# Performance work log

Measured on AMD Instinct MI355X. Metric: run time of the kernel, lower is better.

Reference implementation:

```python
import jax, jax.numpy as jnp
import numpy as np

B, N, C_IN = 2, 2048, 256
H, C_H = 8, 32  # no_heads, c_hidden; H*C_H == 256


def setup_inputs() -> dict:
    key = jax.random.key(0)
    ks = jax.random.split(key, 10)
    s_in = 1.0 / np.sqrt(C_IN)
    s_hid = 1.0 / np.sqrt(H * C_H)
    return {
        "q_x": jax.random.normal(ks[0], (B, N, C_IN), dtype=jnp.float32),
        "kv_x": jax.random.normal(ks[1], (B, N, C_IN), dtype=jnp.float32),
        "bias": jax.random.normal(ks[2], (B, H, N, N), dtype=jnp.float32),
        # Linear weights stored as [in, out] (transpose of torch layout)
        "Wq": jax.random.normal(ks[3], (C_IN, H * C_H), dtype=jnp.float32) * s_in,
        "Wk": jax.random.normal(ks[4], (C_IN, H * C_H), dtype=jnp.float32) * s_in,
        "Wv": jax.random.normal(ks[5], (C_IN, H * C_H), dtype=jnp.float32) * s_in,
        "Wg": jax.random.normal(ks[6], (C_IN, H * C_H), dtype=jnp.float32) * s_in,
        "bg": jnp.zeros((H * C_H,), dtype=jnp.float32),
        "Wo": jax.random.normal(ks[7], (H * C_H, C_IN), dtype=jnp.float32) * s_hid,
        "bo": jnp.zeros((C_IN,), dtype=jnp.float32),
    }


def reference(q_x, kv_x, bias, Wq, Wk, Wv, Wg, bg, Wo, bo):
    inv_sqrt = 1.0 / jnp.sqrt(jnp.asarray(C_H, q_x.dtype))
    # projections -> [B, N, H, C_H]
    q = (q_x @ Wq).reshape(B, N, H, C_H) * inv_sqrt
    k = (kv_x @ Wk).reshape(B, N, H, C_H)
    v = (kv_x @ Wv).reshape(B, N, H, C_H)
    # attention scores [B, H, Nq, Nk] with added pairwise bias
    a = jnp.einsum("bqhc,bkhc->bhqk", q, k) + bias
    a = jax.nn.softmax(a, axis=-1)
    o = jnp.einsum("bhqk,bkhc->bqhc", a, v)  # [B, N, H, C_H]
    # sigmoid gating
    g = jax.nn.sigmoid(q_x @ Wg + bg).reshape(B, N, H, C_H)
    o = o * g
    # output projection
    return o.reshape(B, N, H * C_H) @ Wo + bo
```

## Files before the change

kernel.cpp:

```cpp
#include <hip/hip_runtime.h>
#include <hip/hip_bf16.h>

#define B_   2
#define N_   2048
#define CIN  256
#define NH   8
#define CH   32

typedef unsigned short u16;
typedef __attribute__((ext_vector_type(4))) float f32x4;
typedef __bf16 bf16x8 __attribute__((ext_vector_type(8)));
typedef u16 u16x4 __attribute__((ext_vector_type(4)));
typedef u16 u16x8 __attribute__((ext_vector_type(8)));

static __device__ __forceinline__ u16 b16(float f) {
    __bf16 h = (__bf16)f;
    union { __bf16 h; u16 u; } c; c.h = h; return c.u;
}
static __device__ __forceinline__ float bf2f(u16 u) {
    union { unsigned u; float f; } c; c.u = ((unsigned)u) << 16; return c.f;
}
static __device__ __forceinline__ float sigmoidf_(float x) {
    return 1.0f / (1.0f + __expf(-x));
}
static __device__ __forceinline__ void gload_lds16(const void* g, void* lds) {
    __builtin_amdgcn_global_load_lds(
        (const __attribute__((address_space(1))) unsigned int*)g,
        (__attribute__((address_space(3))) unsigned int*)lds, 16, 0, 0);
}

#define LDW 136

static __device__ __forceinline__ u16x8 cvt8(float4 a, float4 b) {
    u16x8 o;
    o[0] = b16(a.x); o[1] = b16(a.y); o[2] = b16(a.z); o[3] = b16(a.w);
    o[4] = b16(b.x); o[5] = b16(b.y); o[6] = b16(b.z); o[7] = b16(b.w);
    return o;
}
static __device__ __forceinline__ void stg_b16(const u16* __restrict__ src, u16 (*dst)[LDW], int tid) {
#pragma unroll
    for (int i = 0; i < 4; i++) {
        const int e = tid + 256 * i, row = e >> 4, c = e & 15;
        *(bf16x8*)&dst[row][c * 8] = *(const bf16x8*)(src + (size_t)row * CIN + c * 8);
    }
}
static __device__ __forceinline__ void ld1_b16(const u16* __restrict__ src, bf16x8 r[4], int tid) {
#pragma unroll
    for (int i = 0; i < 4; i++) {
        const int e = tid + 256 * i, row = e >> 4, c = e & 15;
        r[i] = *(const bf16x8*)(src + (size_t)row * CIN + 128 + c * 8);
    }
}
static __device__ __forceinline__ void wr1_b16(const bf16x8 r[4], u16 (*dst)[LDW], int tid) {
#pragma unroll
    for (int i = 0; i < 4; i++) {
        const int e = tid + 256 * i, row = e >> 4, c = e & 15;
        *(bf16x8*)&dst[row][c * 8] = r[i];
    }
}
static __device__ __forceinline__ void stg_f32(const float* __restrict__ src, u16 (*dst)[LDW], int tid) {
#pragma unroll
    for (int i = 0; i < 4; i++) {
        const int e = tid + 256 * i, row = e >> 4, c = e & 15;
        const float* s = src + (size_t)row * CIN + c * 8;
        *(u16x8*)&dst[row][c * 8] = cvt8(*(const float4*)s, *(const float4*)(s + 4));
    }
}
static __device__ __forceinline__ void trn_stage(const float* __restrict__ W, int n0,
                                                 u16 (*dst)[LDW], int tid, int kbase, float s) {
#pragma unroll
    for (int i = 0; i < 8; i++) {
        const int e = tid + 256 * i;
        const int kl = e >> 4, nb = e & 15;
#pragma unroll
        for (int j = 0; j < 4; j++) {
            float v = W[(size_t)(kbase + kl) * CIN + n0 + nb + j * 16];
            dst[nb + j * 16][kl] = b16(v * s);
        }
    }
}
static __device__ __forceinline__ void compute_phase(
    const u16 (*At)[LDW], const u16 (*Bt)[LDW], int w, int lr, int lq, f32x4 acc[4])
{
#pragma unroll
    for (int kk = 0; kk < 128; kk += 32) {
        bf16x8 af = *(const bf16x8*)&At[w * 16 + lr][kk + lq * 8];
#pragma unroll
        for (int nt = 0; nt < 4; nt++) {
            bf16x8 bf = *(const bf16x8*)&Bt[nt * 16 + lr][kk + lq * 8];
            acc[nt] = __builtin_amdgcn_mfma_f32_16x16x32_bf16(af, bf, acc[nt], 0, 0, 0);
        }
    }
}

__global__ __launch_bounds__(256, 4)
void proj_kernel(const float* __restrict__ qx, const float* __restrict__ kvx,
                 const float* __restrict__ Wq, const float* __restrict__ Wk,
                 const float* __restrict__ Wv, const float* __restrict__ Wg,
                 const float* __restrict__ bgv, const float* __restrict__ Wo,
                 u16* __restrict__ Qw, u16* __restrict__ Kw,
                 u16* __restrict__ Vt, u16* __restrict__ Gw,
                 u16* __restrict__ WoT)
{
    const int flat = blockIdx.x;
    const int tid = threadIdx.x, w = tid >> 6, l = tid & 63, lr = l & 15, lq = l >> 4;
    __shared__ union {
        float T[64][65];
        struct { u16 At[64][LDW]; u16 Bt[64][LDW]; } g;
    } sh;

    if (flat >= 1024) {
        const int t16 = flat - 1024;
        const int k0 = (t16 & 3) * 64, n0 = (t16 >> 2) * 64;
        const int a = tid >> 4, c4 = (tid & 15) * 4;
#pragma unroll
        for (int i = 0; i < 4; i++) {
            float4 v = *(const float4*)&Wo[(size_t)(k0 + a + i * 16) * CIN + n0 + c4];
            sh.T[a + i * 16][c4 + 0] = v.x; sh.T[a + i * 16][c4 + 1] = v.y;
            sh.T[a + i * 16][c4 + 2] = v.z; sh.T[a + i * 16][c4 + 3] = v.w;
        }
        __syncthreads();
#pragma unroll
        for (int i = 0; i < 4; i++) {
            const int nr = a + i * 16;
            u16x4 o;
            o[0] = b16(sh.T[c4 + 0][nr]); o[1] = b16(sh.T[c4 + 1][nr]);
            o[2] = b16(sh.T[c4 + 2][nr]); o[3] = b16(sh.T[c4 + 3][nr]);
            *(u16x4*)&WoT[(size_t)(n0 + nr) * CIN + k0 + c4] = o;
        }
        return;
    }

    const int z = flat >> 8, y = (flat >> 2) & 63, x = flat & 3;
    const float* Xf = ((z == 0 || z == 3) ? qx : kvx) + (size_t)(y * 64) * CIN;
    const float* Wz = (z == 0) ? Wq : (z == 1) ? Wk : (z == 2) ? Wv : Wg;
    const float scale = (z == 0) ? 0.17677669529663687f : 1.0f;
    const int n0w = x * 64;
    u16 (*Xt)[LDW] = (z == 2) ? sh.g.Bt : sh.g.At;
    u16 (*Wt)[LDW] = (z == 2) ? sh.g.At : sh.g.Bt;

    f32x4 acc[4] = {{0,0,0,0},{0,0,0,0},{0,0,0,0},{0,0,0,0}};

    stg_f32(Xf, Xt, tid);
    trn_stage(Wz, n0w, Wt, tid, 0, scale);
    __syncthreads();
    float4 rx[8];
#pragma unroll
    for (int i = 0; i < 4; i++) {
        const int e = tid + 256 * i, row = e >> 4, c = e & 15;
        const float* s = Xf + (size_t)row * CIN + 128 + c * 8;
        rx[2 * i] = *(const float4*)s; rx[2 * i + 1] = *(const float4*)(s + 4);
    }
    compute_phase(sh.g.At, sh.g.Bt, w, lr, lq, acc);
    __syncthreads();
#pragma unroll
    for (int i = 0; i < 4; i++) {
        const int e = tid + 256 * i, row = e >> 4, c = e & 15;
        *(u16x8*)&Xt[row][c * 8] = cvt8(rx[2 * i], rx[2 * i + 1]);
    }
    trn_stage(Wz, n0w, Wt, tid, 128, scale);
    __syncthreads();
    compute_phase(sh.g.At, sh.g.Bt, w, lr, lq, acc);

    if (z != 2) {
        const int m0 = y * 64 + w * 16, n0 = x * 64;
        if (z == 3) {
#pragma unroll
            for (int nt = 0; nt < 4; nt++) {
                const int col = n0 + nt * 16 + lr;
                const float bb = bgv[col];
#pragma unroll
                for (int r = 0; r < 4; r++)
                    Gw[(size_t)(m0 + lq * 4 + r) * CIN + col] = b16(sigmoidf_(acc[nt][r] + bb));
            }
        } else {
            u16* D = (z == 0) ? Qw : Kw;
#pragma unroll
            for (int nt = 0; nt < 4; nt++)
#pragma unroll
                for (int r = 0; r < 4; r++)
                    D[(size_t)(m0 + lq * 4 + r) * CIN + n0 + nt * 16 + lr] = b16(acc[nt][r]);
        }
    } else {
        const int c0 = x * 64 + w * 16;
        const int n0g = y * 64;
        const int bb_ = n0g >> 11, nl0 = n0g & (N_ - 1);
#pragma unroll
        for (int nt = 0; nt < 4; nt++)
#pragma unroll
            for (int r = 0; r < 4; r++)
                Vt[((size_t)bb_ * CIN + c0 + lq * 4 + r) * N_ + nl0 + nt * 16 + lr] = b16(acc[nt][r]);
    }
}

#define RMAX(x) { x = fmaxf(x, __shfl_xor(x, 1)); x = fmaxf(x, __shfl_xor(x, 2)); \
                  x = fmaxf(x, __shfl_xor(x, 4)); x = fmaxf(x, __shfl_xor(x, 8)); }
#define RSUM(x) { x += __shfl_xor(x, 1); x += __shfl_xor(x, 2); \
                  x += __shfl_xor(x, 4); x += __shfl_xor(x, 8); }

__global__ __launch_bounds__(256)
void attn_kernel(const u16* __restrict__ Qw, const u16* __restrict__ Kw,
                 const u16* __restrict__ Vt, const float* __restrict__ bias,
                 const u16* __restrict__ Gw, u16* __restrict__ Owg)
{
    const int bid = blockIdx.x;
    const int h = bid & 7, qt = (bid >> 3) & 63, b = bid >> 9;
    const int tid = threadIdx.x;
    const int w = tid >> 6, l = tid & 63, lr = l & 15, lq = l >> 4;
    const int rp = w & 1, kh = w >> 1;
    const int qb = qt * 32;

    __shared__ __align__(16) float Btl[4][3][16][32];
    __shared__ u16 Plds[4][8][4][16];

    const bf16x8 qf = *(const bf16x8*)(Qw + (size_t)(b * N_ + qb + rp * 16 + lr) * CIN + h * CH + lq * 8);
    const u16* Kb = Kw + (size_t)(b * N_ + kh * 1024 + lr) * CIN + h * CH + lq * 8;
    const u16* Vb = Vt + (size_t)((b * NH + h) * CH + lr) * N_ + kh * 1024 + lq * 8;
    const float* biasW = bias + ((size_t)(b * NH + h) * N_ + qb + rp * 16) * N_ + kh * 1024;

    const int brow0 = l >> 3;
    const int cswz = ((l & 7) ^ (((l >> 3) & 4) ? 4 : 0)) * 4;
    const float* gl0 = biasW + (size_t)brow0 * N_ + cswz;
    const float* gl1 = biasW + (size_t)(8 + brow0) * N_ + cswz;

#define STAGE(TT, BI) { \
    gload_lds16(gl0 + (size_t)(TT) * 32, &Btl[w][BI][0][0]); \
    gload_lds16(gl1 + (size_t)(TT) * 32, &Btl[w][BI][8][0]); }

#define KVLOAD(K) { kf0 = *(const bf16x8*)(Kb + (size_t)(K) * CIN); \
                    kf1 = *(const bf16x8*)(Kb + (size_t)((K) + 16) * CIN); \
                    vf0 = *(const bf16x8*)(Vb + (K)); \
                    vf1 = *(const bf16x8*)(Vb + 16 * N_ + (K)); }

    f32x4 acc0 = {0.f, 0.f, 0.f, 0.f}, acc1 = {0.f, 0.f, 0.f, 0.f};
    float m0v = 8.f, m1v = 8.f, m2v = 8.f, m3v = 8.f;
    float l0 = 0.f, l1 = 0.f, l2 = 0.f, l3 = 0.f;
    bf16x8 kf0, kf1, vf0, vf1;

    STAGE(0, 0)
    __builtin_amdgcn_sched_barrier(0);
    KVLOAD(0)
    __builtin_amdgcn_sched_barrier(0);
    STAGE(1, 1)
    __builtin_amdgcn_sched_barrier(0);

    const int lrx = lr ^ ((lq & 1) << 4);
    int cur = 0, nxt = 2;
    for (int t = 0; t < 32; t++) {
        asm volatile("s_waitcnt vmcnt(2)" ::: "memory");
        const bf16x8 ck0 = kf0, ck1 = kf1, cv0 = vf0, cv1 = vf1;
        KVLOAD(((t + 1) & 31) * 32)
        __builtin_amdgcn_sched_barrier(0);
        STAGE((t + 2) & 31, nxt)
        __builtin_amdgcn_sched_barrier(0);

        const float* bt = &Btl[w][cur][lq * 4][0];
        f32x4 c0, c1;
        c0[0] = bt[0 * 32 + lrx];        c0[1] = bt[1 * 32 + lrx];
        c0[2] = bt[2 * 32 + lrx];        c0[3] = bt[3 * 32 + lrx];
        c1[0] = bt[0 * 32 + (lrx ^ 16)]; c1[1] = bt[1 * 32 + (lrx ^ 16)];
        c1[2] = bt[2 * 32 + (lrx ^ 16)]; c1[3] = bt[3 * 32 + (lrx ^ 16)];

        f32x4 s0 = __builtin_amdgcn_mfma_f32_16x16x32_bf16(qf, ck0, c0, 0, 0, 0);
        f32x4 s1 = __builtin_amdgcn_mfma_f32_16x16x32_bf16(qf, ck1, c1, 0, 0, 0);

        float pm0 = fmaxf(s0[0], s1[0]);
        float pm1 = fmaxf(s0[1], s1[1]);
        float pm2 = fmaxf(s0[2], s1[2]);
        float pm3 = fmaxf(s0[3], s1[3]);
        bool ev = (pm0 > m0v) || (pm1 > m1v) || (pm2 > m2v) || (pm3 > m3v);
        if (__any(ev)) {
            RMAX(pm0) RMAX(pm1) RMAX(pm2) RMAX(pm3)
            float t0 = fmaxf(m0v, pm0), t1 = fmaxf(m1v, pm1);
            float t2 = fmaxf(m2v, pm2), t3 = fmaxf(m3v, pm3);
            float sc0 = __expf(m0v - t0), sc1 = __expf(m1v - t1);
            float sc2 = __expf(m2v - t2), sc3 = __expf(m3v - t3);
            m0v = t0; m1v = t1; m2v = t2; m3v = t3;
            l0 *= sc0; l1 *= sc1; l2 *= sc2; l3 *= sc3;
            acc0[0] *= sc0; acc0[1] *= sc1; acc0[2] *= sc2; acc0[3] *= sc3;
            acc1[0] *= sc0; acc1[1] *= sc1; acc1[2] *= sc2; acc1[3] *= sc3;
        }
        float p00 = __expf(s0[0] - m0v), p01 = __expf(s0[1] - m1v);
        float p02 = __expf(s0[2] - m2v), p03 = __expf(s0[3] - m3v);
        float p10 = __expf(s1[0] - m0v), p11 = __expf(s1[1] - m1v);
        float p12 = __expf(s1[2] - m2v), p13 = __expf(s1[3] - m3v);
        l0 += p00 + p10; l1 += p01 + p11; l2 += p02 + p12; l3 += p03 + p13;

        u16* pw = &Plds[w][0][lq][lr];
        pw[0 * 64] = b16(p00); pw[1 * 64] = b16(p01);
        pw[2 * 64] = b16(p02); pw[3 * 64] = b16(p03);
        pw[4 * 64] = b16(p10); pw[5 * 64] = b16(p11);
        pw[6 * 64] = b16(p12); pw[7 * 64] = b16(p13);

        const bf16x8 pa = *(const bf16x8*)&Plds[w][(lq >> 1) * 4 + (lr & 3)][lr >> 2][(lq & 1) * 8];
        acc0 = __builtin_amdgcn_mfma_f32_16x16x32_bf16(pa, cv0, acc0, 0, 0, 0);
        acc1 = __builtin_amdgcn_mfma_f32_16x16x32_bf16(pa, cv1, acc1, 0, 0, 0);

        cur = (cur == 2) ? 0 : cur + 1;
        nxt = (nxt == 2) ? 0 : nxt + 1;
    }
#undef STAGE
#undef KVLOAD

    RSUM(l0) RSUM(l1) RSUM(l2) RSUM(l3)

    asm volatile("s_waitcnt vmcnt(0)" ::: "memory");
    float* P = (float*)&Btl[w][0][0][0];
    if (kh == 1) {
#pragma unroll
        for (int r = 0; r < 4; r++) {
            const int row = lq * 4 + r;
            P[row * 32 + lr]      = acc0[r];
            P[row * 32 + 16 + lr] = acc1[r];
        }
        if (lr == 0) {
            P[512 + lq * 4 + 0] = m0v; P[512 + lq * 4 + 1] = m1v;
            P[512 + lq * 4 + 2] = m2v; P[512 + lq * 4 + 3] = m3v;
            P[528 + lq * 4 + 0] = l0;  P[528 + lq * 4 + 1] = l1;
            P[528 + lq * 4 + 2] = l2;  P[528 + lq * 4 + 3] = l3;
        }
    }
    __syncthreads();
    if (kh == 1) return;

    const float* PB = (const float*)&Btl[w + 2][0][0][0];
    const float mA[4] = {m0v, m1v, m2v, m3v};
    const float lA[4] = {l0, l1, l2, l3};

    const u16* Gb = Gw + (size_t)(b * N_ + qb + rp * 16 + lq * 4) * CIN + h * CH + lr;
    u16* Ob = Owg + (size_t)(b * N_ + qb + rp * 16 + lq * 4) * CIN + h * CH + lr;
#pragma unroll
    for (int r = 0; r < 4; r++) {
        const int row = lq * 4 + r;
        const float mB = PB[512 + row];
        const float lB = PB[528 + row];
        const float ob0 = PB[row * 32 + lr];
        const float ob1 = PB[row * 32 + 16 + lr];
        const float mM = fmaxf(mA[r], mB);
        const float sA = __expf(mA[r] - mM), sB = __expf(mB - mM);
        const float rr = 1.0f / (lA[r] * sA + lB * sB);
        const float a0 = (r == 0 ? acc0[0] : r == 1 ? acc0[1] : r == 2 ? acc0[2] : acc0[3]);
        const float a1 = (r == 0 ? acc1[0] : r == 1 ? acc1[1] : r == 2 ? acc1[2] : acc1[3]);
        const float g0 = bf2f(Gb[r * CIN]), g1 = bf2f(Gb[r * CIN + 16]);
        Ob[r * CIN]      = b16((a0 * sA + ob0 * sB) * rr * g0);
        Ob[r * CIN + 16] = b16((a1 * sA + ob1 * sB) * rr * g1);
    }
}

__global__ __launch_bounds__(256, 4)
void out_mfma(const u16* __restrict__ Owg, const u16* __restrict__ WoT,
              const float* __restrict__ bo, float* __restrict__ out)
{
    const int tid = threadIdx.x, w = tid >> 6, l = tid & 63, lr = l & 15, lq = l >> 4;
    const int m0 = blockIdx.y * 64 + w * 16, n0 = blockIdx.x * 64;

    __shared__ u16 At[64][LDW];
    __shared__ u16 Bt[64][LDW];

    const u16* Arows = Owg + (size_t)(blockIdx.y * 64) * CIN;
    const u16* Brows = WoT + (size_t)(blockIdx.x * 64) * CIN;

    f32x4 acc[4] = {{0,0,0,0},{0,0,0,0},{0,0,0,0},{0,0,0,0}};

    stg_b16(Arows, At, tid);
    stg_b16(Brows, Bt, tid);
    __syncthreads();
    bf16x8 ra[4], rb[4];
    ld1_b16(Arows, ra, tid);
    ld1_b16(Brows, rb, tid);
    compute_phase(At, Bt, w, lr, lq, acc);
    __syncthreads();
    wr1_b16(ra, At, tid);
    wr1_b16(rb, Bt, tid);
    __syncthreads();
    compute_phase(At, Bt, w, lr, lq, acc);

#pragma unroll
    for (int nt = 0; nt < 4; nt++) {
        const float bb = bo[n0 + nt * 16 + lr];
#pragma unroll
        for (int r = 0; r < 4; r++)
            out[(size_t)(m0 + lq * 4 + r) * CIN + n0 + nt * 16 + lr] = acc[nt][r] + bb;
    }
}

extern "C" void kernel_launch(void* const* d_in, const int* in_sizes, int n_in,
                              void* d_out, int out_size, void* d_ws, size_t ws_size,
                              hipStream_t stream)
{
    const float* qx   = (const float*)d_in[0];
    const float* kvx  = (const float*)d_in[1];
    const float* bias = (const float*)d_in[2];
    const float* Wq = (const float*)d_in[3];
    const float* Wk = (const float*)d_in[4];
    const float* Wv = (const float*)d_in[5];
    const float* Wg = (const float*)d_in[6];
    const float* bg = (const float*)d_in[7];
    const float* Wo = (const float*)d_in[8];
    const float* bo = (const float*)d_in[9];
    float* out = (float*)d_out;

    char* ws = (char*)d_ws;
    const size_t SZB = (size_t)B_ * N_ * CIN * 2;
    u16* Qw   = (u16*)(ws + 2 * SZB);
    u16* Kw   = (u16*)(ws + 3 * SZB);
    u16* Vt   = (u16*)(ws + 4 * SZB);
    u16* Gw   = (u16*)(ws + 5 * SZB);
    u16* Owg  = (u16*)(ws + 6 * SZB);
    const size_t WSZ = (size_t)CIN * CIN * 2;
    u16* WoT  = (u16*)(ws + 7 * SZB + 4 * WSZ);

    proj_kernel<<<dim3(1040), 256, 0, stream>>>(qx, kvx, Wq, Wk, Wv, Wg, bg, Wo,
                                                Qw, Kw, Vt, Gw, WoT);
    attn_kernel<<<dim3(1024), 256, 0, stream>>>(Qw, Kw, Vt, bias, Gw, Owg);
    out_mfma<<<dim3(4, 64, 1), 256, 0, stream>>>(Owg, WoT, bo, out);
}
```

Measured before the change: 118.5 us.

## Pre-transpose weights in a prep kernel and load attention bias directly into registers

Adds a small prep kernel that transposes and converts all five weight matrices to bf16 once, so the projection kernel stages bf16 weight tiles with vector loads instead of doing a strided scalar transpose in every block. The attention kernel drops async global-to-LDS bias staging with its manual waitcnt and instead loads bias straight into registers, using a 4-way unrolled register ring for bias and double-buffered K/V prefetch. This adds one kernel launch and more live registers in the attention loop, and the bias register loads are scalar and strided.

```diff
diff --git a/kernel.cpp b/kernel.cpp
--- a/kernel.cpp
+++ b/kernel.cpp
@@ -23,11 +23,6 @@
 static __device__ __forceinline__ float sigmoidf_(float x) {
     return 1.0f / (1.0f + __expf(-x));
 }
-static __device__ __forceinline__ void gload_lds16(const void* g, void* lds) {
-    __builtin_amdgcn_global_load_lds(
-        (const __attribute__((address_space(1))) unsigned int*)g,
-        (__attribute__((address_space(3))) unsigned int*)lds, 16, 0, 0);
-}
 
 #define LDW 136
 
@@ -66,19 +61,6 @@
         *(u16x8*)&dst[row][c * 8] = cvt8(*(const float4*)s, *(const float4*)(s + 4));
     }
 }
-static __device__ __forceinline__ void trn_stage(const float* __restrict__ W, int n0,
-                                                 u16 (*dst)[LDW], int tid, int kbase, float s) {
-#pragma unroll
-    for (int i = 0; i < 8; i++) {
-        const int e = tid + 256 * i;
-        const int kl = e >> 4, nb = e & 15;
-#pragma unroll
-        for (int j = 0; j < 4; j++) {
-            float v = W[(size_t)(kbase + kl) * CIN + n0 + nb + j * 16];
-            dst[nb + j * 16][kl] = b16(v * s);
-        }
-    }
-}
 static __device__ __forceinline__ void compute_phase(
     const u16 (*At)[LDW], const u16 (*Bt)[LDW], int w, int lr, int lq, f32x4 acc[4])
 {
@@ -93,77 +75,83 @@
     }
 }
 
+__global__ __launch_bounds__(256)
+void prep80(const float* __restrict__ Wq, const float* __restrict__ Wk,
+            const float* __restrict__ Wv, const float* __restrict__ Wg,
+            const float* __restrict__ Wo,
+            u16* __restrict__ WqT, u16* __restrict__ WkT,
+            u16* __restrict__ WvT, u16* __restrict__ WgT,
+            u16* __restrict__ WoT)
+{
+    const int wz = blockIdx.x;
+    const int tid = threadIdx.x;
+    const int z = wz >> 4, t16 = wz & 15;
+    const int k0 = (t16 & 3) * 64, n0 = (t16 >> 2) * 64;
+    const float* W = (z == 0) ? Wq : (z == 1) ? Wk : (z == 2) ? Wv : (z == 3) ? Wg : Wo;
+    u16* Wt = (z == 0) ? WqT : (z == 1) ? WkT : (z == 2) ? WvT : (z == 3) ? WgT : WoT;
+    const float s = (z == 0) ? 0.17677669529663687f : 1.0f;
+
+    __shared__ float T[64][65];
+    const int a = tid >> 4, c4 = (tid & 15) * 4;
+#pragma unroll
+    for (int i = 0; i < 4; i++) {
+        float4 v = *(const float4*)&W[(size_t)(k0 + a + i * 16) * CIN + n0 + c4];
+        T[a + i * 16][c4 + 0] = v.x * s; T[a + i * 16][c4 + 1] = v.y * s;
+        T[a + i * 16][c4 + 2] = v.z * s; T[a + i * 16][c4 + 3] = v.w * s;
+    }
+    __syncthreads();
+#pragma unroll
+    for (int i = 0; i < 4; i++) {
+        const int nr = a + i * 16;
+        u16x4 o;
+        o[0] = b16(T[c4 + 0][nr]); o[1] = b16(T[c4 + 1][nr]);
+        o[2] = b16(T[c4 + 2][nr]); o[3] = b16(T[c4 + 3][nr]);
+        *(u16x4*)&Wt[(size_t)(n0 + nr) * CIN + k0 + c4] = o;
+    }
+}
+
 __global__ __launch_bounds__(256, 4)
-void proj_kernel(const float* __restrict__ qx, const float* __restrict__ kvx,
-                 const float* __restrict__ Wq, const float* __restrict__ Wk,
-                 const float* __restrict__ Wv, const float* __restrict__ Wg,
-                 const float* __restrict__ bgv, const float* __restrict__ Wo,
-                 u16* __restrict__ Qw, u16* __restrict__ Kw,
-                 u16* __restrict__ Vt, u16* __restrict__ Gw,
-                 u16* __restrict__ WoT)
-{
-    const int flat = blockIdx.x;
+void proj_mfma(const float* __restrict__ qx, const float* __restrict__ kvx,
+               const u16* __restrict__ WqT, const u16* __restrict__ WkT,
+               const u16* __restrict__ WvT, const u16* __restrict__ WgT,
+               const float* __restrict__ bgv,
+               u16* __restrict__ Qw, u16* __restrict__ Kw,
+               u16* __restrict__ Vt, u16* __restrict__ Gw)
+{
+    const int z = blockIdx.z;
     const int tid = threadIdx.x, w = tid >> 6, l = tid & 63, lr = l & 15, lq = l >> 4;
-    __shared__ union {
-        float T[64][65];
-        struct { u16 At[64][LDW]; u16 Bt[64][LDW]; } g;
-    } sh;
-
-    if (flat >= 1024) {
-        const int t16 = flat - 1024;
-        const int k0 = (t16 & 3) * 64, n0 = (t16 >> 2) * 64;
-        const int a = tid >> 4, c4 = (tid & 15) * 4;
+
+    __shared__ u16 At[64][LDW];
+    __shared__ u16 Bt[64][LDW];
+
+    f32x4 acc[4] = {{0,0,0,0},{0,0,0,0},{0,0,0,0},{0,0,0,0}};
+
+    if (z != 2) {
+        const float* Af = ((z == 1) ? kvx : qx) + (size_t)(blockIdx.y * 64) * CIN;
+        const u16*   Bb = ((z == 0) ? WqT : (z == 1) ? WkT : WgT) + (size_t)(blockIdx.x * 64) * CIN;
+        stg_f32(Af, At, tid);
+        stg_b16(Bb, Bt, tid);
+        __syncthreads();
+        float4 raf[8]; bf16x8 rb[4];
 #pragma unroll
         for (int i = 0; i < 4; i++) {
-            float4 v = *(const float4*)&Wo[(size_t)(k0 + a + i * 16) * CIN + n0 + c4];
-            sh.T[a + i * 16][c4 + 0] = v.x; sh.T[a + i * 16][c4 + 1] = v.y;
-            sh.T[a + i * 16][c4 + 2] = v.z; sh.T[a + i * 16][c4 + 3] = v.w;
-        }
+            const int e = tid + 256 * i, row = e >> 4, c = e & 15;
+            const float* s = Af + (size_t)row * CIN + 128 + c * 8;
+            raf[2 * i] = *(const float4*)s; raf[2 * i + 1] = *(const float4*)(s + 4);
+        }
+        ld1_b16(Bb, rb, tid);
+        compute_phase(At, Bt, w, lr, lq, acc);
         __syncthreads();
 #pragma unroll
         for (int i = 0; i < 4; i++) {
-            const int nr = a + i * 16;
-            u16x4 o;
-            o[0] = b16(sh.T[c4 + 0][nr]); o[1] = b16(sh.T[c4 + 1][nr]);
-            o[2] = b16(sh.T[c4 + 2][nr]); o[3] = b16(sh.T[c4 + 3][nr]);
-            *(u16x4*)&WoT[(size_t)(n0 + nr) * CIN + k0 + c4] = o;
-        }
-        return;
-    }
-
-    const int z = flat >> 8, y = (flat >> 2) & 63, x = flat & 3;
-    const float* Xf = ((z == 0 || z == 3) ? qx : kvx) + (size_t)(y * 64) * CIN;
-    const float* Wz = (z == 0) ? Wq : (z == 1) ? Wk : (z == 2) ? Wv : Wg;
-    const float scale = (z == 0) ? 0.17677669529663687f : 1.0f;
-    const int n0w = x * 64;
-    u16 (*Xt)[LDW] = (z == 2) ? sh.g.Bt : sh.g.At;
-    u16 (*Wt)[LDW] = (z == 2) ? sh.g.At : sh.g.Bt;
-
-    f32x4 acc[4] = {{0,0,0,0},{0,0,0,0},{0,0,0,0},{0,0,0,0}};
-
-    stg_f32(Xf, Xt, tid);
-    trn_stage(Wz, n0w, Wt, tid, 0, scale);
-    __syncthreads();
-    float4 rx[8];
-#pragma unroll
-    for (int i = 0; i < 4; i++) {
-        const int e = tid + 256 * i, row = e >> 4, c = e & 15;
-        const float* s = Xf + (size_t)row * CIN + 128 + c * 8;
-        rx[2 * i] = *(const float4*)s; rx[2 * i + 1] = *(const float4*)(s + 4);
-    }
-    compute_phase(sh.g.At, sh.g.Bt, w, lr, lq, acc);
-    __syncthreads();
-#pragma unroll
-    for (int i = 0; i < 4; i++) {
-        const int e = tid + 256 * i, row = e >> 4, c = e & 15;
-        *(u16x8*)&Xt[row][c * 8] = cvt8(rx[2 * i], rx[2 * i + 1]);
-    }
-    trn_stage(Wz, n0w, Wt, tid, 128, scale);
-    __syncthreads();
-    compute_phase(sh.g.At, sh.g.Bt, w, lr, lq, acc);
-
-    if (z != 2) {
-        const int m0 = y * 64 + w * 16, n0 = x * 64;
+            const int e = tid + 256 * i, row = e >> 4, c = e & 15;
+            *(u16x8*)&At[row][c * 8] = cvt8(raf[2 * i], raf[2 * i + 1]);
+        }
+        wr1_b16(rb, Bt, tid);
+        __syncthreads();
+        compute_phase(At, Bt, w, lr, lq, acc);
+
+        const int m0 = blockIdx.y * 64 + w * 16, n0 = blockIdx.x * 64;
         if (z == 3) {
 #pragma unroll
             for (int nt = 0; nt < 4; nt++) {
@@ -182,8 +170,32 @@
                     D[(size_t)(m0 + lq * 4 + r) * CIN + n0 + nt * 16 + lr] = b16(acc[nt][r]);
         }
     } else {
-        const int c0 = x * 64 + w * 16;
-        const int n0g = y * 64;
+        const u16*   Ab = WvT + (size_t)(blockIdx.x * 64) * CIN;
+        const float* Bf = kvx + (size_t)(blockIdx.y * 64) * CIN;
+        stg_b16(Ab, At, tid);
+        stg_f32(Bf, Bt, tid);
+        __syncthreads();
+        bf16x8 ra[4]; float4 rbf[8];
+        ld1_b16(Ab, ra, tid);
+#pragma unroll
+        for (int i = 0; i < 4; i++) {
+            const int e = tid + 256 * i, row = e >> 4, c = e & 15;
+            const float* s = Bf + (size_t)row * CIN + 128 + c * 8;
+            rbf[2 * i] = *(const float4*)s; rbf[2 * i + 1] = *(const float4*)(s + 4);
+        }
+        compute_phase(At, Bt, w, lr, lq, acc);
+        __syncthreads();
+        wr1_b16(ra, At, tid);
+#pragma unroll
+        for (int i = 0; i < 4; i++) {
+            const int e = tid + 256 * i, row = e >> 4, c = e & 15;
+            *(u16x8*)&Bt[row][c * 8] = cvt8(rbf[2 * i], rbf[2 * i + 1]);
+        }
+        __syncthreads();
+        compute_phase(At, Bt, w, lr, lq, acc);
+
+        const int c0 = blockIdx.x * 64 + w * 16;
+        const int n0g = blockIdx.y * 64;
         const int bb_ = n0g >> 11, nl0 = n0g & (N_ - 1);
 #pragma unroll
         for (int nt = 0; nt < 4; nt++)
@@ -210,102 +222,95 @@
     const int rp = w & 1, kh = w >> 1;
     const int qb = qt * 32;
 
-    __shared__ __align__(16) float Btl[4][3][16][32];
+    __shared__ float Mrg[2][544];
     __shared__ u16 Plds[4][8][4][16];
 
     const bf16x8 qf = *(const bf16x8*)(Qw + (size_t)(b * N_ + qb + rp * 16 + lr) * CIN + h * CH + lq * 8);
     const u16* Kb = Kw + (size_t)(b * N_ + kh * 1024 + lr) * CIN + h * CH + lq * 8;
     const u16* Vb = Vt + (size_t)((b * NH + h) * CH + lr) * N_ + kh * 1024 + lq * 8;
-    const float* biasW = bias + ((size_t)(b * NH + h) * N_ + qb + rp * 16) * N_ + kh * 1024;
-
-    const int brow0 = l >> 3;
-    const int cswz = ((l & 7) ^ (((l >> 3) & 4) ? 4 : 0)) * 4;
-    const float* gl0 = biasW + (size_t)brow0 * N_ + cswz;
-    const float* gl1 = biasW + (size_t)(8 + brow0) * N_ + cswz;
-
-#define STAGE(TT, BI) { \
-    gload_lds16(gl0 + (size_t)(TT) * 32, &Btl[w][BI][0][0]); \
-    gload_lds16(gl1 + (size_t)(TT) * 32, &Btl[w][BI][8][0]); }
-
-#define KVLOAD(K) { kf0 = *(const bf16x8*)(Kb + (size_t)(K) * CIN); \
-                    kf1 = *(const bf16x8*)(Kb + (size_t)((K) + 16) * CIN); \
-                    vf0 = *(const bf16x8*)(Vb + (K)); \
-                    vf1 = *(const bf16x8*)(Vb + 16 * N_ + (K)); }
+    const float* bW = bias + ((size_t)(b * NH + h) * N_ + qb + rp * 16) * N_ + kh * 1024;
+    const float* bR0 = bW + (size_t)(lq * 4) * N_ + lr;
+    const float* bR1 = bR0 + N_;
+    const float* bR2 = bR1 + N_;
+    const float* bR3 = bR2 + N_;
+
+#define BLOAD(T, BA, BB) { \
+    const int co_ = (T) * 32; \
+    BA[0] = bR0[co_];      BA[1] = bR1[co_];      BA[2] = bR2[co_];      BA[3] = bR3[co_]; \
+    BB[0] = bR0[co_ + 16]; BB[1] = bR1[co_ + 16]; BB[2] = bR2[co_ + 16]; BB[3] = bR3[co_ + 16]; }
+
+#define KVLOAD(K, K0, K1, V0, V1) { \
+    K0 = *(const bf16x8*)(Kb + (size_t)(K) * CIN); \
+    K1 = *(const bf16x8*)(Kb + (size_t)((K) + 16) * CIN); \
+    V0 = *(const bf16x8*)(Vb + (K)); \
+    V1 = *(const bf16x8*)(Vb + 16 * N_ + (K)); }
 
     f32x4 acc0 = {0.f, 0.f, 0.f, 0.f}, acc1 = {0.f, 0.f, 0.f, 0.f};
     float m0v = 8.f, m1v = 8.f, m2v = 8.f, m3v = 8.f;
     float l0 = 0.f, l1 = 0.f, l2 = 0.f, l3 = 0.f;
-    bf16x8 kf0, kf1, vf0, vf1;
-
-    STAGE(0, 0)
+    f32x4 bA0, bB0, bA1, bB1, bA2, bB2, bA3, bB3;
+    bf16x8 ka0, ka1, va0, va1, kb0, kb1, vb0, vb1;
+
+    BLOAD(0, bA0, bB0)
+    KVLOAD(0, ka0, ka1, va0, va1)
+    BLOAD(1, bA1, bB1)
+    KVLOAD(32, kb0, kb1, vb0, vb1)
+    BLOAD(2, bA2, bB2)
     __builtin_amdgcn_sched_barrier(0);
-    KVLOAD(0)
-    __builtin_amdgcn_sched_barrier(0);
-    STAGE(1, 1)
-    __builtin_amdgcn_sched_barrier(0);
-
-    const int lrx = lr ^ ((lq & 1) << 4);
-    int cur = 0, nxt = 2;
-    for (int t = 0; t < 32; t++) {
-        asm volatile("s_waitcnt vmcnt(2)" ::: "memory");
-        const bf16x8 ck0 = kf0, ck1 = kf1, cv0 = vf0, cv1 = vf1;
-        KVLOAD(((t + 1) & 31) * 32)
-        __builtin_amdgcn_sched_barrier(0);
-        STAGE((t + 2) & 31, nxt)
-        __builtin_amdgcn_sched_barrier(0);
-
-        const float* bt = &Btl[w][cur][lq * 4][0];
-        f32x4 c0, c1;
-        c0[0] = bt[0 * 32 + lrx];        c0[1] = bt[1 * 32 + lrx];
-        c0[2] = bt[2 * 32 + lrx];        c0[3] = bt[3 * 32 + lrx];
-        c1[0] = bt[0 * 32 + (lrx ^ 16)]; c1[1] = bt[1 * 32 + (lrx ^ 16)];
-        c1[2] = bt[2 * 32 + (lrx ^ 16)]; c1[3] = bt[3 * 32 + (lrx ^ 16)];
-
-        f32x4 s0 = __builtin_amdgcn_mfma_f32_16x16x32_bf16(qf, ck0, c0, 0, 0, 0);
-        f32x4 s1 = __builtin_amdgcn_mfma_f32_16x16x32_bf16(qf, ck1, c1, 0, 0, 0);
-
-        float pm0 = fmaxf(s0[0], s1[0]);
-        float pm1 = fmaxf(s0[1], s1[1]);
-        float pm2 = fmaxf(s0[2], s1[2]);
-        float pm3 = fmaxf(s0[3], s1[3]);
-        bool ev = (pm0 > m0v) || (pm1 > m1v) || (pm2 > m2v) || (pm3 > m3v);
-        if (__any(ev)) {
-            RMAX(pm0) RMAX(pm1) RMAX(pm2) RMAX(pm3)
-            float t0 = fmaxf(m0v, pm0), t1 = fmaxf(m1v, pm1);
-            float t2 = fmaxf(m2v, pm2), t3 = fmaxf(m3v, pm3);
-            float sc0 = __expf(m0v - t0), sc1 = __expf(m1v - t1);
-            float sc2 = __expf(m2v - t2), sc3 = __expf(m3v - t3);
-            m0v = t0; m1v = t1; m2v = t2; m3v = t3;
-            l0 *= sc0; l1 *= sc1; l2 *= sc2; l3 *= sc3;
-            acc0[0] *= sc0; acc0[1] *= sc1; acc0[2] *= sc2; acc0[3] *= sc3;
-            acc1[0] *= sc0; acc1[1] *= sc1; acc1[2] *= sc2; acc1[3] *= sc3;
-        }
-        float p00 = __expf(s0[0] - m0v), p01 = __expf(s0[1] - m1v);
-        float p02 = __expf(s0[2] - m2v), p03 = __expf(s0[3] - m3v);
-        float p10 = __expf(s1[0] - m0v), p11 = __expf(s1[1] - m1v);
-        float p12 = __expf(s1[2] - m2v), p13 = __expf(s1[3] - m3v);
-        l0 += p00 + p10; l1 += p01 + p11; l2 += p02 + p12; l3 += p03 + p13;
-
-        u16* pw = &Plds[w][0][lq][lr];
-        pw[0 * 64] = b16(p00); pw[1 * 64] = b16(p01);
-        pw[2 * 64] = b16(p02); pw[3 * 64] = b16(p03);
-        pw[4 * 64] = b16(p10); pw[5 * 64] = b16(p11);
-        pw[6 * 64] = b16(p12); pw[7 * 64] = b16(p13);
-
-        const bf16x8 pa = *(const bf16x8*)&Plds[w][(lq >> 1) * 4 + (lr & 3)][lr >> 2][(lq & 1) * 8];
-        acc0 = __builtin_amdgcn_mfma_f32_16x16x32_bf16(pa, cv0, acc0, 0, 0, 0);
-        acc1 = __builtin_amdgcn_mfma_f32_16x16x32_bf16(pa, cv1, acc1, 0, 0, 0);
-
-        cur = (cur == 2) ? 0 : cur + 1;
-        nxt = (nxt == 2) ? 0 : nxt + 1;
-    }
-#undef STAGE
+
+#define TBODY(t, BA, BB, NBA, NBB, K0, K1, V0, V1) { \
+    const bf16x8 ck0 = K0, ck1 = K1, cv0 = V0, cv1 = V1; \
+    f32x4 c0, c1; \
+    c0[0] = BA[0]; c0[1] = BA[1]; c0[2] = BA[2]; c0[3] = BA[3]; \
+    c1[0] = BB[0]; c1[1] = BB[1]; c1[2] = BB[2]; c1[3] = BB[3]; \
+    KVLOAD((((t) + 2) & 31) * 32, K0, K1, V0, V1) \
+    BLOAD(((t) + 3) & 31, NBA, NBB) \
+    __builtin_amdgcn_sched_barrier(0); \
+    f32x4 s0 = __builtin_amdgcn_mfma_f32_16x16x32_bf16(qf, ck0, c0, 0, 0, 0); \
+    f32x4 s1 = __builtin_amdgcn_mfma_f32_16x16x32_bf16(qf, ck1, c1, 0, 0, 0); \
+    float pm0 = fmaxf(s0[0], s1[0]); \
+    float pm1 = fmaxf(s0[1], s1[1]); \
+    float pm2 = fmaxf(s0[2], s1[2]); \
+    float pm3 = fmaxf(s0[3], s1[3]); \
+    bool ev = (pm0 > m0v) || (pm1 > m1v) || (pm2 > m2v) || (pm3 > m3v); \
+    if (__any(ev)) { \
+        RMAX(pm0) RMAX(pm1) RMAX(pm2) RMAX(pm3) \
+        float t0 = fmaxf(m0v, pm0), t1 = fmaxf(m1v, pm1); \
+        float t2 = fmaxf(m2v, pm2), t3 = fmaxf(m3v, pm3); \
+        float sc0 = __expf(m0v - t0), sc1 = __expf(m1v - t1); \
+        float sc2 = __expf(m2v - t2), sc3 = __expf(m3v - t3); \
+        m0v = t0; m1v = t1; m2v = t2; m3v = t3; \
+        l0 *= sc0; l1 *= sc1; l2 *= sc2; l3 *= sc3; \
+        acc0[0] *= sc0; acc0[1] *= sc1; acc0[2] *= sc2; acc0[3] *= sc3; \
+        acc1[0] *= sc0; acc1[1] *= sc1; acc1[2] *= sc2; acc1[3] *= sc3; \
+    } \
+    float p00 = __expf(s0[0] - m0v), p01 = __expf(s0[1] - m1v); \
+    float p02 = __expf(s0[2] - m2v), p03 = __expf(s0[3] - m3v); \
+    float p10 = __expf(s1[0] - m0v), p11 = __expf(s1[1] - m1v); \
+    float p12 = __expf(s1[2] - m2v), p13 = __expf(s1[3] - m3v); \
+    l0 += p00 + p10; l1 += p01 + p11; l2 += p02 + p12; l3 += p03 + p13; \
+    u16* pw = &Plds[w][0][lq][lr]; \
+    pw[0 * 64] = b16(p00); pw[1 * 64] = b16(p01); \
+    pw[2 * 64] = b16(p02); pw[3 * 64] = b16(p03); \
+    pw[4 * 64] = b16(p10); pw[5 * 64] = b16(p11); \
+    pw[6 * 64] = b16(p12); pw[7 * 64] = b16(p13); \
+    const bf16x8 pa = *(const bf16x8*)&Plds[w][(lq >> 1) * 4 + (lr & 3)][lr >> 2][(lq & 1) * 8]; \
+    acc0 = __builtin_amdgcn_mfma_f32_16x16x32_bf16(pa, cv0, acc0, 0, 0, 0); \
+    acc1 = __builtin_amdgcn_mfma_f32_16x16x32_bf16(pa, cv1, acc1, 0, 0, 0); }
+
+    for (int tt = 0; tt < 8; ++tt) {
+        TBODY(tt * 4 + 0, bA0, bB0, bA3, bB3, ka0, ka1, va0, va1)
+        TBODY(tt * 4 + 1, bA1, bB1, bA0, bB0, kb0, kb1, vb0, vb1)
+        TBODY(tt * 4 + 2, bA2, bB2, bA1, bB1, ka0, ka1, va0, va1)
+        TBODY(tt * 4 + 3, bA3, bB3, bA2, bB2, kb0, kb1, vb0, vb1)
+    }
+#undef TBODY
+#undef BLOAD
 #undef KVLOAD
 
     RSUM(l0) RSUM(l1) RSUM(l2) RSUM(l3)
 
-    asm volatile("s_waitcnt vmcnt(0)" ::: "memory");
-    float* P = (float*)&Btl[w][0][0][0];
+    float* P = Mrg[rp];
     if (kh == 1) {
 #pragma unroll
         for (int r = 0; r < 4; r++) {
@@ -323,7 +328,6 @@
     __syncthreads();
     if (kh == 1) return;
 
-    const float* PB = (const float*)&Btl[w + 2][0][0][0];
     const float mA[4] = {m0v, m1v, m2v, m3v};
     const float lA[4] = {l0, l1, l2, l3};
 
@@ -332,10 +336,10 @@
 #pragma unroll
     for (int r = 0; r < 4; r++) {
         const int row = lq * 4 + r;
-        const float mB = PB[512 + row];
-        const float lB = PB[528 + row];
-        const float ob0 = PB[row * 32 + lr];
-        const float ob1 = PB[row * 32 + 16 + lr];
+        const float mB = P[512 + row];
+        const float lB = P[528 + row];
+        const float ob0 = P[row * 32 + lr];
+        const float ob1 = P[row * 32 + 16 + lr];
         const float mM = fmaxf(mA[r], mB);
         const float sA = __expf(mA[r] - mM), sB = __expf(mB - mM);
         const float rr = 1.0f / (lA[r] * sA + lB * sB);
@@ -408,10 +412,16 @@
     u16* Gw   = (u16*)(ws + 5 * SZB);
     u16* Owg  = (u16*)(ws + 6 * SZB);
     const size_t WSZ = (size_t)CIN * CIN * 2;
-    u16* WoT  = (u16*)(ws + 7 * SZB + 4 * WSZ);
-
-    proj_kernel<<<dim3(1040), 256, 0, stream>>>(qx, kvx, Wq, Wk, Wv, Wg, bg, Wo,
-                                                Qw, Kw, Vt, Gw, WoT);
+    u16* WqT = (u16*)(ws + 7 * SZB + 0 * WSZ);
+    u16* WkT = (u16*)(ws + 7 * SZB + 1 * WSZ);
+    u16* WvT = (u16*)(ws + 7 * SZB + 2 * WSZ);
+    u16* WgT = (u16*)(ws + 7 * SZB + 3 * WSZ);
+    u16* WoT = (u16*)(ws + 7 * SZB + 4 * WSZ);
+
+    prep80<<<dim3(80), 256, 0, stream>>>(Wq, Wk, Wv, Wg, Wo,
+                                         WqT, WkT, WvT, WgT, WoT);
+    proj_mfma<<<dim3(4, 64, 4), 256, 0, stream>>>(qx, kvx, WqT, WkT, WvT, WgT,
+                                                  bg, Qw, Kw, Vt, Gw);
     attn_kernel<<<dim3(1024), 256, 0, stream>>>(Qw, Kw, Vt, bias, Gw, Owg);
     out_mfma<<<dim3(4, 64, 1), 256, 0, stream>>>(Owg, WoT, bo, out);
 }
```

New measurement: 123.5 us. 4.2% more time.
